# Performance work log

Measured on AMD Instinct MI355X. Metric: run time of the kernel, lower is better.

The kernel has to match this reference:

```python
import jax, jax.numpy as jnp
import numpy as np

SIGMA = 10.0


def setup_inputs() -> dict:
    key = jax.random.key(0)
    k1, k2 = jax.random.split(key)
    B, C, K, D = 1024, 1000, 4, 1024
    f = jax.random.normal(k1, (B, D), dtype=jnp.float32)
    # kaiming_normal_ on (C, K, D): fan_in = K*D, std = sqrt(2/fan_in)
    std = np.sqrt(2.0 / (K * D)).astype(np.float32)
    centers = jax.random.normal(k2, (C, K, D), dtype=jnp.float32) * std
    return {"f": f, "centers": centers}


def reference(f, centers):
    B, D = f.shape
    C, K, _ = centers.shape
    mc = C * K
    w = centers.reshape(mc, D)  # [mc, D]

    # ||f - w||^2 = |f|^2 + |w|^2 - 2 f.w  (avoids [B,C,K,D] broadcast tensor)
    f_sq = jnp.sum(f * f, axis=-1, keepdims=True)            # [B, 1]
    w_sq = jnp.sum(w * w, axis=-1)                           # [mc]
    fw = f @ w.T                                             # [B, mc] GEMM
    fw_norm = jnp.maximum(f_sq + w_sq[None, :] - 2.0 * fw, 0.0)
    distance = jnp.exp(-fw_norm / SIGMA).reshape(B, C, K)
    distance = jnp.max(distance, axis=-1)                    # [B, C]

    # pairwise center regularization
    ww = w @ w.T                                             # [mc, mc]
    w_norm_mat = jnp.maximum(w_sq[:, None] + w_sq[None, :] - 2.0 * ww, 0.0)
    w_norm_upper = jnp.triu(w_norm_mat)
    denom = 2.0 / (mc * mc - mc)
    mu = denom * jnp.sum(w_norm_upper)
    residuals = jnp.triu((w_norm_upper - mu) ** 2)
    rw = denom * jnp.sum(residuals)

    rw_broadcast = jnp.ones((B, 1), dtype=f.dtype) * rw
    return jnp.concatenate((distance, rw_broadcast), axis=-1)  # [B, C+1]
```

## Files before the change

### kernel.cpp

```cpp
#include <hip/hip_runtime.h>

#define BB 1024
#define CC 1000
#define DD 1024
#define MC 4000
#define MCP 4096
#define SIGMA_INV (1.0f/10.0f)
#define NT 16
#define NIT 8

typedef __attribute__((ext_vector_type(8))) short bf16x8;
typedef __attribute__((ext_vector_type(4))) float f32x4;

#define GLDS16(g, l) __builtin_amdgcn_global_load_lds( \
    (const __attribute__((address_space(1))) void*)(g), \
    (__attribute__((address_space(3))) void*)(l), 16, 0, 0)

#define SBAR()   __builtin_amdgcn_s_barrier()
#define SCHED()  __builtin_amdgcn_sched_barrier(0)
#define PRIO(x)  __builtin_amdgcn_s_setprio(x)

__device__ __forceinline__ unsigned short f2bf(float x) {
  unsigned u = __float_as_uint(x);
  unsigned r = (u + 0x7fffu + ((u >> 16) & 1u)) >> 16;
  return (unsigned short)r;
}

__global__ __launch_bounds__(256) void prep_kernel(
    const float* __restrict__ f, const float* __restrict__ centers,
    unsigned short* __restrict__ fbf, unsigned short* __restrict__ wbf,
    float* __restrict__ f_sq, float* __restrict__ w_sq,
    double* __restrict__ acc2)
{
  if (blockIdx.x == 0 && threadIdx.x == 0) { acc2[0] = 0.0; acc2[1] = 0.0; }
  const int wv = threadIdx.x >> 6, lane = threadIdx.x & 63;
  const int row = blockIdx.x * 4 + wv;
  const float* src = nullptr;
  unsigned short* dst;
  float* sqp;
  if (row < BB) {
    src = f + (size_t)row * DD; dst = fbf + (size_t)row * DD; sqp = f_sq + row;
  } else {
    int wr = row - BB;
    dst = wbf + (size_t)wr * DD; sqp = w_sq + wr;
    if (wr < MC) src = centers + (size_t)wr * DD;
  }
  float ssum = 0.f;
#pragma unroll
  for (int p = 0; p < 4; ++p) {
    int idx = p * 256 + lane * 4;
    float4 v = make_float4(0.f, 0.f, 0.f, 0.f);
    if (src) v = *(const float4*)(src + idx);
    ssum += v.x * v.x + v.y * v.y + v.z * v.z + v.w * v.w;
    ushort4 o;
    o.x = f2bf(v.x); o.y = f2bf(v.y); o.z = f2bf(v.z); o.w = f2bf(v.w);
    *(ushort4*)(dst + idx) = o;
  }
#pragma unroll
  for (int s = 32; s; s >>= 1) ssum += __shfl_xor(ssum, s);
  if (lane == 0) *sqp = ssum;
}


#define STAGE(SET, AB, SRC, K0, H) do { \
  GLDS16((SRC) + (K0) + soff[(H)*2+0], &lds[SET][AB][doff[(H)*2+0]]); \
  GLDS16((SRC) + (K0) + soff[(H)*2+1], &lds[SET][AB][doff[(H)*2+1]]); \
} while(0)

#define READ_A(SET, MH) do { \
  _Pragma("unroll") for (int ks = 0; ks < 2; ++ks) \
  _Pragma("unroll") for (int m = 0; m < 4; ++m) { \
    int row = wr*128 + ((MH)*4 + m)*16 + rlo; \
    int slot = (ks*4 + rhi) ^ rx; \
    af[ks][m] = *(const bf16x8*)&lds[SET][0][row*64 + slot*8]; \
  } } while(0)

#define READ_B(SET, NH, BW) do { \
  _Pragma("unroll") for (int ks = 0; ks < 2; ++ks) \
  _Pragma("unroll") for (int n = 0; n < 2; ++n) { \
    int row = wc*64 + ((NH)*2 + n)*16 + rlo; \
    int slot = (ks*4 + rhi) ^ rx; \
    BW[ks][n] = *(const bf16x8*)&lds[SET][1][row*64 + slot*8]; \
  } } while(0)

#define MFMA_Q(MH, NH, BW) do { \
  _Pragma("unroll") for (int ks = 0; ks < 2; ++ks) \
  _Pragma("unroll") for (int m = 0; m < 4; ++m) \
  _Pragma("unroll") for (int n = 0; n < 2; ++n) \
    acc[(MH)*4+m][(NH)*2+n] = __builtin_amdgcn_mfma_f32_16x16x32_bf16( \
        af[ks][m], BW[ks][n], acc[(MH)*4+m][(NH)*2+n], 0, 0, 0); \
} while(0)

#define PHASE_MID() do { SCHED(); SBAR(); SCHED(); PRIO(1); } while(0)
#define PHASE_END() do { PRIO(0); SCHED(); SBAR(); SCHED(); } while(0)

__global__ __launch_bounds__(512, 2) void gemm_kernel(
    const unsigned short* __restrict__ fbf, const unsigned short* __restrict__ wbf,
    const float* __restrict__ f_sq, const float* __restrict__ w_sq,
    float* __restrict__ out, double* __restrict__ acc2)
{
  __shared__ __align__(16) unsigned short lds[2][2][256 * 64];

  const int tid = threadIdx.x;
  const int lane = tid & 63, wv = tid >> 6;
  const int wr = wv >> 2, wc = wv & 3;
  const int rlo = lane & 15, rhi = lane >> 4, rx = lane & 7;

  const int orig = blockIdx.x;
  const int bid = (orig & 7) * 25 + (orig >> 3);
  const bool is_fw = bid < 64;
  int tr, tc;
  const unsigned short* Abase;
  if (is_fw) {
    tr = bid >> 4; tc = bid & 15;
    Abase = fbf;
  } else {
    int t = bid - 64;
    tr = 0;
    while (t >= 16 - tr) { t -= 16 - tr; ++tr; }
    tc = tr + t;
    Abase = wbf;
  }
  const unsigned short* Arow = Abase + (size_t)tr * 256 * DD;
  const unsigned short* Brow = wbf  + (size_t)tc * 256 * DD;

  int soff[4], doff[4];
#pragma unroll
  for (int h = 0; h < 2; ++h)
#pragma unroll
    for (int i = 0; i < 2; ++i) {
      int idx = h * 1024 + i * 512 + tid;
      int drow = idx >> 3, dslot = idx & 7;
      int schunk = dslot ^ (drow & 7);
      soff[h * 2 + i] = drow * DD + schunk * 8;
      doff[h * 2 + i] = idx * 8;
    }

  f32x4 acc[8][4] = {};
  bf16x8 af[2][4], bw0[2][2], bw1[2][2];

  STAGE(0, 0, Arow, 0, 0);
  STAGE(0, 0, Arow, 0, 1);
  STAGE(0, 1, Brow, 0, 0);
  STAGE(0, 1, Brow, 0, 1);
  STAGE(1, 1, Brow, 64, 0);
  STAGE(1, 1, Brow, 64, 1);
  SCHED();
  asm volatile("s_waitcnt vmcnt(4)" ::: "memory");
  SCHED();
  SBAR();
  SCHED();

#pragma unroll 1
  for (int it = 0; it < NIT; ++it) {
    const int ka  = (2 * it + 1) * 64;
    const int kb0 = (2 * it + 2) * 64;
    const int kb1 = (2 * it + 3) * 64;
    const bool st = (it < NIT - 1);

    READ_A(0, 0); READ_B(0, 0, bw0);
    STAGE(1, 0, Arow, ka, 0);
    PHASE_MID(); MFMA_Q(0, 0, bw0); PHASE_END();

    READ_B(0, 1, bw1);
    STAGE(1, 0, Arow, ka, 1);
    PHASE_MID(); MFMA_Q(0, 1, bw1); PHASE_END();

    READ_A(0, 1);
    if (st) STAGE(0, 1, Brow, kb0, 0);
    PHASE_MID(); MFMA_Q(1, 1, bw1); PHASE_END();

    if (st) STAGE(0, 1, Brow, kb0, 1);
    PHASE_MID(); MFMA_Q(1, 0, bw0);
    PRIO(0); SCHED();
    if (st) asm volatile("s_waitcnt vmcnt(4)" ::: "memory");
    else    asm volatile("s_waitcnt vmcnt(0)" ::: "memory");
    SCHED(); SBAR(); SCHED();

    READ_A(1, 0); READ_B(1, 0, bw0);
    if (st) STAGE(0, 0, Arow, kb0, 0);
    PHASE_MID(); MFMA_Q(0, 0, bw0); PHASE_END();

    READ_B(1, 1, bw1);
    if (st) STAGE(0, 0, Arow, kb0, 1);
    PHASE_MID(); MFMA_Q(0, 1, bw1); PHASE_END();

    READ_A(1, 1);
    if (st) STAGE(1, 1, Brow, kb1, 0);
    PHASE_MID(); MFMA_Q(1, 1, bw1); PHASE_END();

    if (st) STAGE(1, 1, Brow, kb1, 1);
    PHASE_MID(); MFMA_Q(1, 0, bw0);
    PRIO(0); SCHED();
    asm volatile("s_waitcnt vmcnt(4)" ::: "memory");
    SCHED(); SBAR(); SCHED();
  }

  if (is_fw) {
#pragma unroll
    for (int mf = 0; mf < 8; ++mf) {
      int row = tr * 256 + wr * 128 + mf * 16 + rhi * 4;
#pragma unroll
      for (int nf = 0; nf < 4; ++nf) {
        int col = tc * 256 + wc * 64 + nf * 16 + rlo;
        float wsq = w_sq[col];
#pragma unroll
        for (int r = 0; r < 4; ++r) {
          float fn = f_sq[row + r] + wsq - 2.0f * acc[mf][nf][r];
          fn = fmaxf(fn, 0.f);
          float dist = __expf(-fn * SIGMA_INV);
          dist = fmaxf(dist, __shfl_xor(dist, 1));
          dist = fmaxf(dist, __shfl_xor(dist, 2));
          if ((lane & 3) == 0 && col < MC)
            out[(size_t)(row + r) * (CC + 1) + (col >> 2)] = dist;
        }
      }
    }
  } else {
    double s1 = 0.0, s2 = 0.0;
#pragma unroll
    for (int mf = 0; mf < 8; ++mf) {
      int i0 = tr * 256 + wr * 128 + mf * 16 + rhi * 4;
#pragma unroll
      for (int nf = 0; nf < 4; ++nf) {
        int j = tc * 256 + wc * 64 + nf * 16 + rlo;
        float wsqj = (j < MC) ? w_sq[j] : 0.f;
#pragma unroll
        for (int r = 0; r < 4; ++r) {
          int i = i0 + r;
          if (i < MC && j < MC && j >= i) {
            float s = fmaxf(w_sq[i] + wsqj - 2.0f * acc[mf][nf][r], 0.f);
            s1 += (double)s;
            double d = (double)s - 1.0;
            s2 += d * d;
          }
        }
      }
    }
#pragma unroll
    for (int s = 32; s; s >>= 1) { s1 += __shfl_xor(s1, s); s2 += __shfl_xor(s2, s); }
    double* rbuf = (double*)&lds[0][0][0];
    if (lane == 0) { rbuf[wv] = s1; rbuf[8 + wv] = s2; }
    __syncthreads();
    if (tid == 0) {
      double t1 = 0.0, t2 = 0.0;
#pragma unroll
      for (int w = 0; w < 8; ++w) { t1 += rbuf[w]; t2 += rbuf[8 + w]; }
      atomicAdd(&acc2[0], t1);
      atomicAdd(&acc2[1], t2);
    }
  }
}

__global__ __launch_bounds__(256) void finalize_kernel(
    const double* __restrict__ acc2, float* __restrict__ out)
{
  __shared__ float rws;
  if (threadIdx.x == 0) {
    double SS1 = acc2[0], SS2 = acc2[1];
    double denom = 2.0 / ((double)MC * (double)MC - (double)MC);
    double mu = denom * SS1;
    double T = (double)MC * (double)(MC + 1) * 0.5;
    double sm1 = SS1 - T;
    double dm = mu - 1.0;
    double resid = SS2 - 2.0 * dm * sm1 + T * dm * dm;
    rws = (float)(denom * resid);
  }
  __syncthreads();
  float v = rws;
  for (int b = threadIdx.x; b < BB; b += 256)
    out[(size_t)b * (CC + 1) + CC] = v;
}

extern "C" void kernel_launch(void* const* d_in, const int* in_sizes, int n_in,
                              void* d_out, int out_size, void* d_ws, size_t ws_size,
                              hipStream_t stream) {
  const float* f = (const float*)d_in[0];
  const float* centers = (const float*)d_in[1];
  float* out = (float*)d_out;
  char* ws = (char*)d_ws;

  double* acc2        = (double*)(ws + 0);
  float* f_sq         = (float*)(ws + 4096);
  float* w_sq         = (float*)(ws + 8192);
  unsigned short* fbf = (unsigned short*)(ws + 24576);
  unsigned short* wbf = (unsigned short*)(ws + 24576 + 2 * 1024 * 1024);

  prep_kernel<<<(BB + MCP) / 4, 256, 0, stream>>>(f, centers, fbf, wbf, f_sq, w_sq, acc2);
  gemm_kernel<<<200, 512, 0, stream>>>(fbf, wbf, f_sq, w_sq, out, acc2);
  finalize_kernel<<<1, 256, 0, stream>>>(acc2, out);
}
```

Before: 117.0 us.

## Replace ping-pong phased schedule with simple double-buffered K loop

```diff
diff --git a/kernel.cpp b/kernel.cpp
--- a/kernel.cpp
+++ b/kernel.cpp
@@ -7,7 +7,6 @@
 #define MCP 4096
 #define SIGMA_INV (1.0f/10.0f)
 #define NT 16
-#define NIT 8
 
 typedef __attribute__((ext_vector_type(8))) short bf16x8;
 typedef __attribute__((ext_vector_type(4))) float f32x4;
@@ -91,9 +90,6 @@
         af[ks][m], BW[ks][n], acc[(MH)*4+m][(NH)*2+n], 0, 0, 0); \
 } while(0)
 
-#define PHASE_MID() do { SCHED(); SBAR(); SCHED(); PRIO(1); } while(0)
-#define PHASE_END() do { PRIO(0); SCHED(); SBAR(); SCHED(); } while(0)
-
 __global__ __launch_bounds__(512, 2) void gemm_kernel(
     const unsigned short* __restrict__ fbf, const unsigned short* __restrict__ wbf,
     const float* __restrict__ f_sq, const float* __restrict__ w_sq,
@@ -143,57 +139,44 @@
   STAGE(0, 0, Arow, 0, 1);
   STAGE(0, 1, Brow, 0, 0);
   STAGE(0, 1, Brow, 0, 1);
+  STAGE(1, 0, Arow, 64, 0);
+  STAGE(1, 0, Arow, 64, 1);
   STAGE(1, 1, Brow, 64, 0);
   STAGE(1, 1, Brow, 64, 1);
   SCHED();
-  asm volatile("s_waitcnt vmcnt(4)" ::: "memory");
+  asm volatile("s_waitcnt vmcnt(8)" ::: "memory");
   SCHED();
   SBAR();
   SCHED();
 
-#pragma unroll 1
-  for (int it = 0; it < NIT; ++it) {
-    const int ka  = (2 * it + 1) * 64;
-    const int kb0 = (2 * it + 2) * 64;
-    const int kb1 = (2 * it + 3) * 64;
-    const bool st = (it < NIT - 1);
-
-    READ_A(0, 0); READ_B(0, 0, bw0);
-    STAGE(1, 0, Arow, ka, 0);
-    PHASE_MID(); MFMA_Q(0, 0, bw0); PHASE_END();
-
-    READ_B(0, 1, bw1);
-    STAGE(1, 0, Arow, ka, 1);
-    PHASE_MID(); MFMA_Q(0, 1, bw1); PHASE_END();
-
-    READ_A(0, 1);
-    if (st) STAGE(0, 1, Brow, kb0, 0);
-    PHASE_MID(); MFMA_Q(1, 1, bw1); PHASE_END();
-
-    if (st) STAGE(0, 1, Brow, kb0, 1);
-    PHASE_MID(); MFMA_Q(1, 0, bw0);
-    PRIO(0); SCHED();
-    if (st) asm volatile("s_waitcnt vmcnt(4)" ::: "memory");
-    else    asm volatile("s_waitcnt vmcnt(0)" ::: "memory");
-    SCHED(); SBAR(); SCHED();
-
-    READ_A(1, 0); READ_B(1, 0, bw0);
-    if (st) STAGE(0, 0, Arow, kb0, 0);
-    PHASE_MID(); MFMA_Q(0, 0, bw0); PHASE_END();
-
-    READ_B(1, 1, bw1);
-    if (st) STAGE(0, 0, Arow, kb0, 1);
-    PHASE_MID(); MFMA_Q(0, 1, bw1); PHASE_END();
-
-    READ_A(1, 1);
-    if (st) STAGE(1, 1, Brow, kb1, 0);
-    PHASE_MID(); MFMA_Q(1, 1, bw1); PHASE_END();
-
-    if (st) STAGE(1, 1, Brow, kb1, 1);
-    PHASE_MID(); MFMA_Q(1, 0, bw0);
-    PRIO(0); SCHED();
-    asm volatile("s_waitcnt vmcnt(4)" ::: "memory");
-    SCHED(); SBAR(); SCHED();
+#pragma unroll 2
+  for (int t = 0; t < NT; ++t) {
+    const int set = t & 1;
+
+    READ_A(set, 0); READ_B(set, 0, bw0);
+    PRIO(1);
+    MFMA_Q(0, 0, bw0);
+    READ_B(set, 1, bw1);
+    MFMA_Q(0, 1, bw1);
+    READ_A(set, 1);
+    MFMA_Q(1, 1, bw1);
+    MFMA_Q(1, 0, bw0);
+    PRIO(0);
+
+    if (t < NT - 1) {
+      SCHED(); SBAR(); SCHED();
+      if (t + 2 < NT) {
+        const int k2 = (t + 2) * 64;
+        STAGE(set, 0, Arow, k2, 0);
+        STAGE(set, 0, Arow, k2, 1);
+        STAGE(set, 1, Brow, k2, 0);
+        STAGE(set, 1, Brow, k2, 1);
+      }
+      SCHED();
+      if (t < NT - 2) asm volatile("s_waitcnt vmcnt(8)" ::: "memory");
+      else            asm volatile("s_waitcnt vmcnt(0)" ::: "memory");
+      SCHED(); SBAR(); SCHED();
+    }
   }
 
   if (is_fw) {
```

New measurement: 118.6 us. About the same (+1.4%).
